# Optimization experiments

Hardware: AMD Instinct MI355X
Metric: run time of the kernel (lower is better)

Reference implementation:

```python
import jax, jax.numpy as jnp
import numpy as np

H = 24          # num_heads
QKV = 3 * 3072  # qkv_features * 3
EPS = 1e-6


def apply_rope(q, k, pe):
    # q,k: [B,H,L,D]; pe: [1,1,L,D//2,2,2]
    def rot(t):
        t_ = t.reshape(*t.shape[:-1], -1, 1, 2)  # [B,H,L,D/2,1,2]
        out = pe[..., 0] * t_[..., 0] + pe[..., 1] * t_[..., 1]  # [B,H,L,D/2,2]
        return out.reshape(t.shape)
    return rot(q), rot(k)


def setup_inputs() -> dict:
    key = jax.random.key(0)
    ks = jax.random.split(key, 8)
    B, L, D, Dh = 1, 2048, 3072, 128
    s = lambda n: 1.0 / np.sqrt(n)
    return {
        "x": jax.random.normal(ks[0], (B, L, D), jnp.float32),
        "vec": jax.random.normal(ks[1], (B, D), jnp.float32),
        "pe": jax.random.normal(ks[2], (1, 1, L, Dh // 2, 2, 2), jnp.float32),
        "w_mod": jax.random.normal(ks[3], (D, 3 * D), jnp.float32) * s(D),
        "b_mod": jnp.zeros((3 * D,), jnp.float32),
        "w1": jax.random.normal(ks[4], (D, QKV + 4 * D), jnp.float32) * s(D),
        "b1": jnp.zeros((QKV + 4 * D,), jnp.float32),
        "w2": jax.random.normal(ks[5], (D + 4 * D, D), jnp.float32) * s(5 * D),
        "b2": jnp.zeros((D,), jnp.float32),
        "q_scale": jnp.ones((Dh,), jnp.float32),
        "k_scale": jnp.ones((Dh,), jnp.float32),
    }


def reference(x, vec, pe, w_mod, b_mod, w1, b1, w2, b2, q_scale, k_scale):
    B, L, D = x.shape
    # modulation: silu + linear -> shift, scale, gate each [B,1,D]
    m = jax.nn.silu(vec) @ w_mod + b_mod
    shift, scale, gate = [t[:, None, :] for t in jnp.split(m, 3, axis=-1)]
    # pre-norm (LayerNorm, no scale/bias) + modulate
    mu = jnp.mean(x, axis=-1, keepdims=True)
    var = jnp.mean((x - mu) ** 2, axis=-1, keepdims=True)
    xn = (x - mu) * jax.lax.rsqrt(var + EPS)
    x_mod = (1.0 + scale) * xn + shift
    # fused qkv + mlp projection
    h = x_mod @ w1 + b1
    qkv, mlp = h[..., :QKV], h[..., QKV:]
    qkv = qkv.reshape(B, L, 3, H, -1).transpose(2, 0, 3, 1, 4)  # [3,B,H,L,Dh]
    q, k, v = qkv[0], qkv[1], qkv[2]
    # QK RMSNorm
    rms = lambda t, g: t * jax.lax.rsqrt(jnp.mean(t * t, axis=-1, keepdims=True) + EPS) * g
    q, k = rms(q, q_scale), rms(k, k_scale)
    # RoPE
    q, k = apply_rope(q, k, pe)
    # attention
    Dh = q.shape[-1]
    logits = jnp.einsum("bhqd,bhkd->bhqk", q, k) * (Dh ** -0.5)
    attn = jnp.einsum("bhqk,bhkd->bhqd", jax.nn.softmax(logits, axis=-1), v)
    attn = attn.transpose(0, 2, 1, 3).reshape(B, L, H * Dh)
    # parallel gated MLP + output projection
    out = jnp.concatenate((attn, jax.nn.gelu(mlp)), axis=-1) @ w2 + b2
    return x + gate * out
```

## Files before the change

### kernel.cpp

```cpp
#include <hip/hip_runtime.h>

typedef __bf16 bf16;
typedef __bf16 bf16x8 __attribute__((ext_vector_type(8)));
typedef float f32x4 __attribute__((ext_vector_type(4)));

#define L_SEQ   2048
#define D_MODEL 3072
#define N_HEADS 24
#define N1      21504
#define QKV_N   9216
#define CC      15360


__device__ __forceinline__ void async_cp16(const void* g, void* s) {
    __builtin_amdgcn_global_load_lds((const __attribute__((address_space(1))) void*)g,
                                     (__attribute__((address_space(3))) void*)s, 16, 0, 0);
}

__global__ __launch_bounds__(256) void mod_init_kernel(const float* __restrict__ b_mod, float* __restrict__ m) {
    int j = blockIdx.x * 256 + threadIdx.x;
    m[j] = b_mod[j];
}

__global__ __launch_bounds__(256) void mod_gemv_kernel(const float* __restrict__ vec,
                                                       const float* __restrict__ w_mod,
                                                       float* __restrict__ m) {
    int j  = blockIdx.x * 256 + threadIdx.x;
    int d0 = blockIdx.y * 256;
    __shared__ float sv[256];
    float x = vec[d0 + threadIdx.x];
    sv[threadIdx.x] = x / (1.f + __expf(-x));
    __syncthreads();
    float acc = 0.f;
    #pragma unroll 8
    for (int d = 0; d < 256; d++)
        acc += sv[d] * w_mod[(size_t)(d0 + d) * QKV_N + j];
    atomicAdd(&m[j], acc);
}

__global__ __launch_bounds__(256) void ln_kernel(const float* __restrict__ x,
                                                 const float* __restrict__ m,
                                                 bf16* __restrict__ x_mod) {
    int l = blockIdx.x, tid = threadIdx.x;
    const float4* xr = (const float4*)(x + (size_t)l * D_MODEL);
    float4 v[3];
    float s = 0.f, ss = 0.f;
    #pragma unroll
    for (int p = 0; p < 3; p++) {
        v[p] = xr[p * 256 + tid];
        s  += v[p].x + v[p].y + v[p].z + v[p].w;
        ss += v[p].x * v[p].x + v[p].y * v[p].y + v[p].z * v[p].z + v[p].w * v[p].w;
    }
    #pragma unroll
    for (int off = 32; off; off >>= 1) { s += __shfl_xor(s, off); ss += __shfl_xor(ss, off); }
    __shared__ float rs[4], rss[4];
    int wave = tid >> 6, lane = tid & 63;
    if (lane == 0) { rs[wave] = s; rss[wave] = ss; }
    __syncthreads();
    s  = rs[0] + rs[1] + rs[2] + rs[3];
    ss = rss[0] + rss[1] + rss[2] + rss[3];
    float mu   = s * (1.f / D_MODEL);
    float var  = ss * (1.f / D_MODEL) - mu * mu;
    float rstd = rsqrtf(var + 1e-6f);
    #pragma unroll
    for (int p = 0; p < 3; p++) {
        int c = (p * 256 + tid) * 4;
        const float* ve = (const float*)&v[p];
        union { bf16 b[4]; uint2 u; } pk;
        #pragma unroll
        for (int e = 0; e < 4; e++) {
            float xn = (ve[e] - mu) * rstd;
            pk.b[e] = (bf16)((1.f + m[D_MODEL + c + e]) * xn + m[c + e]);
        }
        *(uint2*)(x_mod + (size_t)l * D_MODEL + c) = pk.u;
    }
}

__global__ __launch_bounds__(256) void tconv_kernel(const float* __restrict__ in, bf16* __restrict__ out,
                                                    int R, int C) {
    __shared__ float T[64][65];
    int c0 = blockIdx.x * 64, r0 = blockIdx.y * 64;
    int tid = threadIdx.x;
    int col4 = (tid & 15) * 4, rr = tid >> 4;
    #pragma unroll
    for (int p = 0; p < 4; p++) {
        int r = rr + p * 16;
        float4 v = *(const float4*)(in + (size_t)(r0 + r) * C + c0 + col4);
        T[r][col4 + 0] = v.x; T[r][col4 + 1] = v.y; T[r][col4 + 2] = v.z; T[r][col4 + 3] = v.w;
    }
    __syncthreads();
    int c = tid >> 2, rq = (tid & 3) * 16;
    union { bf16 b[16]; uint4 u[2]; } pk;
    #pragma unroll
    for (int i = 0; i < 16; i++) pk.b[i] = (bf16)T[rq + i][c];
    uint4* op = (uint4*)(out + (size_t)(c0 + c) * R + r0 + rq);
    op[0] = pk.u[0]; op[1] = pk.u[1];
}

template <int EPI>
__global__ __launch_bounds__(256) void gemm_kernel(
    const bf16* __restrict__ A, const bf16* __restrict__ Bt,
    const float* __restrict__ bias, int K, int ld,
    bf16* __restrict__ o_qkv, bf16* __restrict__ o_concat,
    float* __restrict__ p0, float* __restrict__ p1) {
    __shared__ bf16 As[128 * 32];
    __shared__ bf16 Bs[128 * 32];
    const int tid = threadIdx.x;
    const int wave = tid >> 6, lane = tid & 63;
    const int l16 = lane & 15, lq = lane >> 4;
    const int wm = (wave >> 1) * 64, wn = (wave & 1) * 64;
    const int m0 = blockIdx.y * 128, n0 = blockIdx.x * 128;
    const int koff = (EPI == 2) ? blockIdx.z * K : 0;

    const int srow  = wave * 16 + (lane >> 2);
    const int skoff = (lane & 3) * 8;
    const bf16* Ag = A  + (size_t)(m0 + srow) * ld + koff + skoff;
    const bf16* Bg = Bt + (size_t)(n0 + srow) * ld + koff + skoff;
    bf16* As_w = As + wave * 16 * 32;
    bf16* Bs_w = Bs + wave * 16 * 32;

    f32x4 acc[4][4];
    #pragma unroll
    for (int i = 0; i < 4; i++)
        #pragma unroll
        for (int j = 0; j < 4; j++) acc[i][j] = f32x4{0.f, 0.f, 0.f, 0.f};

    for (int k0 = 0; k0 < K; k0 += 32) {
        __syncthreads();
        async_cp16(Ag + k0,                    As_w);
        async_cp16(Ag + k0 + (size_t)64 * ld,  As_w + 64 * 32);
        async_cp16(Bg + k0,                    Bs_w);
        async_cp16(Bg + k0 + (size_t)64 * ld,  Bs_w + 64 * 32);
        __syncthreads();
        bf16x8 af[4], bfr[4];
        #pragma unroll
        for (int i = 0; i < 4; i++) af[i]  = *(const bf16x8*)(As + (wm + 16 * i + l16) * 32 + lq * 8);
        #pragma unroll
        for (int j = 0; j < 4; j++) bfr[j] = *(const bf16x8*)(Bs + (wn + 16 * j + l16) * 32 + lq * 8);
        #pragma unroll
        for (int i = 0; i < 4; i++)
            #pragma unroll
            for (int j = 0; j < 4; j++)
                acc[i][j] = __builtin_amdgcn_mfma_f32_16x16x32_bf16(af[i], bfr[j], acc[i][j], 0, 0, 0);
    }

    float* po = (EPI == 2) ? (blockIdx.z ? p1 : p0) : nullptr;
    #pragma unroll
    for (int i = 0; i < 4; i++) {
        int row = m0 + wm + 16 * i + lq * 4;
        #pragma unroll
        for (int j = 0; j < 4; j++) {
            int col = n0 + wn + 16 * j + l16;
            float bv = (EPI == 1) ? bias[col] : 0.f;
            #pragma unroll
            for (int r = 0; r < 4; r++) {
                float v = acc[i][j][r] + bv;
                int rr = row + r;
                if (EPI == 1) {
                    if (col < QKV_N) {
                        o_qkv[(size_t)rr * QKV_N + col] = (bf16)v;
                    } else {
                        float g = 0.5f * v * (1.f + tanhf(0.7978845608028654f * (v + 0.044715f * v * v * v)));
                        o_concat[(size_t)rr * CC + (col - QKV_N + D_MODEL)] = (bf16)g;
                    }
                } else {
                    po[(size_t)rr * D_MODEL + col] = v;
                }
            }
        }
    }
}

__global__ __launch_bounds__(256) void res_kernel(const float* __restrict__ p0, const float* __restrict__ p1,
                                                  const float* __restrict__ x, const float* __restrict__ gate,
                                                  const float* __restrict__ b2, float* __restrict__ out) {
    int i = blockIdx.x * 256 + threadIdx.x;
    float4 a  = ((const float4*)p0)[i];
    float4 b  = ((const float4*)p1)[i];
    float4 xr = ((const float4*)x)[i];
    int col = (i * 4) % D_MODEL;
    float4 g  = *(const float4*)(gate + col);
    float4 bb = *(const float4*)(b2 + col);
    float4 o;
    o.x = xr.x + g.x * (a.x + b.x + bb.x);
    o.y = xr.y + g.y * (a.y + b.y + bb.y);
    o.z = xr.z + g.z * (a.z + b.z + bb.z);
    o.w = xr.w + g.w * (a.w + b.w + bb.w);
    ((float4*)out)[i] = o;
}

__global__ __launch_bounds__(256) void qkv_rope_kernel(const bf16* __restrict__ hqkv,
                                                       const float* __restrict__ pe,
                                                       const float* __restrict__ q_scale,
                                                       const float* __restrict__ k_scale,
                                                       bf16* __restrict__ q_r, bf16* __restrict__ k_r) {
    int wave = threadIdx.x >> 6, lane = threadIdx.x & 63;
    int idx = blockIdx.x * 4 + wave;
    int l = idx / N_HEADS, h = idx - l * N_HEADS;
    const bf16* qg = hqkv + (size_t)l * QKV_N + h * 128;
    const bf16* kg = qg + D_MODEL;
    float q0 = (float)qg[2 * lane], q1 = (float)qg[2 * lane + 1];
    float k0 = (float)kg[2 * lane], k1 = (float)kg[2 * lane + 1];
    float sq = q0 * q0 + q1 * q1, sk = k0 * k0 + k1 * k1;
    #pragma unroll
    for (int off = 32; off; off >>= 1) { sq += __shfl_xor(sq, off); sk += __shfl_xor(sk, off); }
    float rq = rsqrtf(sq * (1.f / 128.f) + 1e-6f);
    float rk = rsqrtf(sk * (1.f / 128.f) + 1e-6f);
    float s0 = q_scale[2 * lane], s1 = q_scale[2 * lane + 1];
    float z0 = k_scale[2 * lane], z1 = k_scale[2 * lane + 1];
    float4 p = ((const float4*)pe)[(size_t)l * 64 + lane];
    float tq0 = q0 * rq * s0, tq1 = q1 * rq * s1;
    float tk0 = k0 * rk * z0, tk1 = k1 * rk * z1;
    size_t ob = ((size_t)h * L_SEQ + l) * 128 + 2 * lane;
    q_r[ob]     = (bf16)(p.x * tq0 + p.y * tq1);
    q_r[ob + 1] = (bf16)(p.z * tq0 + p.w * tq1);
    k_r[ob]     = (bf16)(p.x * tk0 + p.y * tk1);
    k_r[ob + 1] = (bf16)(p.z * tk0 + p.w * tk1);
}

__global__ __launch_bounds__(256) void vtrans_kernel(const bf16* __restrict__ hqkv, bf16* __restrict__ v_t) {
    int dt = blockIdx.x * 64, lt = blockIdx.y * 64, h = blockIdx.z;
    __shared__ bf16 T[64][72];
    int tid = threadIdx.x;
    #pragma unroll
    for (int p = 0; p < 2; p++) {
        int idx = p * 256 + tid;
        int r = idx >> 3, c = idx & 7;
        uint4 v = *(const uint4*)(hqkv + (size_t)(lt + r) * QKV_N + 2 * D_MODEL + h * 128 + dt + c * 8);
        *(uint4*)(&T[r][c * 8]) = v;
    }
    __syncthreads();
    #pragma unroll
    for (int p = 0; p < 2; p++) {
        int idx = p * 256 + tid;
        int d = idx >> 3, c = idx & 7;
        union { bf16 b[8]; uint4 u; } pk;
        #pragma unroll
        for (int i = 0; i < 8; i++) pk.b[i] = T[c * 8 + i][d];
        *(uint4*)(v_t + ((size_t)h * 128 + dt + d) * L_SEQ + lt + c * 8) = pk.u;
    }
}

#define QK_LD 136
#define VP_LD 72
__global__ __launch_bounds__(256) void attn_kernel(const bf16* __restrict__ q_r, const bf16* __restrict__ k_r,
                                                   const bf16* __restrict__ v_t, bf16* __restrict__ concat) {
    const int h = blockIdx.y;
    const int q0 = blockIdx.x * 64;
    __shared__ bf16 Qs[64 * QK_LD];
    __shared__ bf16 Ks[64 * QK_LD];
    __shared__ bf16 Vs[128 * VP_LD];
    __shared__ bf16 Ps[64 * VP_LD];
    const int tid = threadIdx.x, wave = tid >> 6, lane = tid & 63;
    const int l16 = lane & 15, lq = lane >> 4;
    const bf16* Qg = q_r + ((size_t)h * L_SEQ + q0) * 128;
    const bf16* Kg = k_r + (size_t)h * L_SEQ * 128;
    const bf16* Vg = v_t + (size_t)h * 128 * L_SEQ;
    #pragma unroll
    for (int p = 0; p < 4; p++) {
        int idx = p * 256 + tid, r = idx >> 4, c = idx & 15;
        *(uint4*)(Qs + r * QK_LD + c * 8) = *(const uint4*)(Qg + (size_t)r * 128 + c * 8);
    }
    f32x4 accO[8];
    #pragma unroll
    for (int i = 0; i < 8; i++) accO[i] = f32x4{0.f, 0.f, 0.f, 0.f};
    float mrow[4] = {-1e30f, -1e30f, -1e30f, -1e30f};
    float lrow[4] = {0.f, 0.f, 0.f, 0.f};
    const float sc = 0.08838834764831845f * 1.4426950408889634f;
    for (int kt = 0; kt < 32; kt++) {
        __syncthreads();
        const bf16* Kt = Kg + (size_t)kt * 64 * 128;
        const bf16* Vt = Vg + kt * 64;
        #pragma unroll
        for (int p = 0; p < 4; p++) {
            int idx = p * 256 + tid, r = idx >> 4, c = idx & 15;
            *(uint4*)(Ks + r * QK_LD + c * 8) = *(const uint4*)(Kt + (size_t)r * 128 + c * 8);
        }
        #pragma unroll
        for (int p = 0; p < 4; p++) {
            int idx = p * 256 + tid, r = idx >> 3, c = idx & 7;
            *(uint4*)(Vs + r * VP_LD + c * 8) = *(const uint4*)(Vt + (size_t)r * L_SEQ + c * 8);
        }
        __syncthreads();
        f32x4 accS[4];
        #pragma unroll
        for (int i = 0; i < 4; i++) accS[i] = f32x4{0.f, 0.f, 0.f, 0.f};
        #pragma unroll
        for (int kk = 0; kk < 4; kk++) {
            bf16x8 a = *(const bf16x8*)(Qs + (wave * 16 + l16) * QK_LD + kk * 32 + lq * 8);
            #pragma unroll
            for (int nt = 0; nt < 4; nt++) {
                bf16x8 b = *(const bf16x8*)(Ks + (nt * 16 + l16) * QK_LD + kk * 32 + lq * 8);
                accS[nt] = __builtin_amdgcn_mfma_f32_16x16x32_bf16(a, b, accS[nt], 0, 0, 0);
            }
        }
        float alpha[4];
        #pragma unroll
        for (int r = 0; r < 4; r++) {
            float x0 = accS[0][r] * sc, x1 = accS[1][r] * sc, x2 = accS[2][r] * sc, x3 = accS[3][r] * sc;
            float mx = fmaxf(fmaxf(x0, x1), fmaxf(x2, x3));
            #pragma unroll
            for (int off = 1; off < 16; off <<= 1) mx = fmaxf(mx, __shfl_xor(mx, off));
            float mnew = fmaxf(mrow[r], mx);
            alpha[r] = __builtin_amdgcn_exp2f(mrow[r] - mnew);
            float p0 = __builtin_amdgcn_exp2f(x0 - mnew), p1 = __builtin_amdgcn_exp2f(x1 - mnew);
            float p2 = __builtin_amdgcn_exp2f(x2 - mnew), p3 = __builtin_amdgcn_exp2f(x3 - mnew);
            float rsum = p0 + p1 + p2 + p3;
            #pragma unroll
            for (int off = 1; off < 16; off <<= 1) rsum += __shfl_xor(rsum, off);
            lrow[r] = lrow[r] * alpha[r] + rsum;
            mrow[r] = mnew;
            int prow = wave * 16 + lq * 4 + r;
            Ps[prow * VP_LD +  0 + l16] = (bf16)p0;
            Ps[prow * VP_LD + 16 + l16] = (bf16)p1;
            Ps[prow * VP_LD + 32 + l16] = (bf16)p2;
            Ps[prow * VP_LD + 48 + l16] = (bf16)p3;
        }
        #pragma unroll
        for (int i = 0; i < 8; i++) {
            accO[i][0] *= alpha[0]; accO[i][1] *= alpha[1];
            accO[i][2] *= alpha[2]; accO[i][3] *= alpha[3];
        }
        #pragma unroll
        for (int kk = 0; kk < 2; kk++) {
            bf16x8 a = *(const bf16x8*)(Ps + (wave * 16 + l16) * VP_LD + kk * 32 + lq * 8);
            #pragma unroll
            for (int nt = 0; nt < 8; nt++) {
                bf16x8 b = *(const bf16x8*)(Vs + (nt * 16 + l16) * VP_LD + kk * 32 + lq * 8);
                accO[nt] = __builtin_amdgcn_mfma_f32_16x16x32_bf16(a, b, accO[nt], 0, 0, 0);
            }
        }
    }
    float inv[4];
    #pragma unroll
    for (int r = 0; r < 4; r++) inv[r] = 1.f / lrow[r];
    #pragma unroll
    for (int nt = 0; nt < 8; nt++)
        #pragma unroll
        for (int r = 0; r < 4; r++) {
            int row = q0 + wave * 16 + lq * 4 + r;
            concat[(size_t)row * CC + h * 128 + nt * 16 + l16] = (bf16)(accO[nt][r] * inv[r]);
        }
}

extern "C" void kernel_launch(void* const* d_in, const int* in_sizes, int n_in,
                              void* d_out, int out_size, void* d_ws, size_t ws_size,
                              hipStream_t stream) {
    const float* x       = (const float*)d_in[0];
    const float* vec     = (const float*)d_in[1];
    const float* pe      = (const float*)d_in[2];
    const float* w_mod   = (const float*)d_in[3];
    const float* b_mod   = (const float*)d_in[4];
    const float* w1      = (const float*)d_in[5];
    const float* b1      = (const float*)d_in[6];
    const float* w2      = (const float*)d_in[7];
    const float* b2      = (const float*)d_in[8];
    const float* q_scale = (const float*)d_in[9];
    const float* k_scale = (const float*)d_in[10];
    float* out = (float*)d_out;

    char* ws = (char*)d_ws;
    float* m_buf  = (float*)(ws);
    bf16* x_mod   = (bf16*)(ws + 36864);
    bf16* w1t     = (bf16*)(ws + 12619776);
    bf16* hqkv    = (bf16*)(ws + 144740352);
    bf16* concat  = (bf16*)(ws + 182489088);
    bf16* q_r     = (bf16*)(ws + 245403648);
    bf16* k_r     = (bf16*)(ws + 257986560);
    bf16* v_t     = (bf16*)(ws + 270569472);
    float* p0     = (float*)(ws + 144740352);
    float* p1     = (float*)(ws + 245403648);

    mod_init_kernel<<<36, 256, 0, stream>>>(b_mod, m_buf);
    mod_gemv_kernel<<<dim3(36, 12), 256, 0, stream>>>(vec, w_mod, m_buf);
    ln_kernel<<<L_SEQ, 256, 0, stream>>>(x, m_buf, x_mod);
    tconv_kernel<<<dim3(N1 / 64, D_MODEL / 64), 256, 0, stream>>>(w1, w1t, D_MODEL, N1);
    gemm_kernel<1><<<dim3(N1 / 128, L_SEQ / 128, 1), 256, 0, stream>>>(
        x_mod, w1t, b1, D_MODEL, D_MODEL, hqkv, concat, nullptr, nullptr);
    qkv_rope_kernel<<<L_SEQ * N_HEADS / 4, 256, 0, stream>>>(hqkv, pe, q_scale, k_scale, q_r, k_r);
    vtrans_kernel<<<dim3(2, 32, N_HEADS), 256, 0, stream>>>(hqkv, v_t);
    attn_kernel<<<dim3(32, N_HEADS), 256, 0, stream>>>(q_r, k_r, v_t, concat);
    tconv_kernel<<<dim3(D_MODEL / 64, CC / 64), 256, 0, stream>>>(w2, w1t, CC, D_MODEL);
    gemm_kernel<2><<<dim3(D_MODEL / 128, L_SEQ / 128, 2), 256, 0, stream>>>(
        concat, w1t, nullptr, CC / 2, CC, nullptr, nullptr, p0, p1);
    res_kernel<<<L_SEQ * D_MODEL / 1024, 256, 0, stream>>>(p0, p1, x, m_buf + 2 * D_MODEL, b2, out);
}
```

Before: 1.449 ms.

## Use 32x32x16 MFMA with BK=64 XOR-swizzled LDS in GEMM; keep Q in registers

The GEMM kernel moves from 16x16x32 to 32x32x16 bf16 MFMA tiles, doubles the K step to 64 and XOR-swizzles the LDS layout to avoid bank conflicts, with launch bounds asking for 3 blocks per CU. The aim is fewer LDS reads per MFMA and half as many barriers per K. Separately, the attention kernel loads its Q fragments straight into registers and drops the Q shared-memory tile. LDS use per GEMM block doubles, and the occupancy hint may force register spills.

```diff
diff --git a/kernel.cpp b/kernel.cpp
--- a/kernel.cpp
+++ b/kernel.cpp
@@ -3,6 +3,7 @@
 typedef __bf16 bf16;
 typedef __bf16 bf16x8 __attribute__((ext_vector_type(8)));
 typedef float f32x4 __attribute__((ext_vector_type(4)));
+typedef float f32x16 __attribute__((ext_vector_type(16)));
 
 #define L_SEQ   2048
 #define D_MODEL 3072
@@ -98,64 +99,71 @@
 }
 
 template <int EPI>
-__global__ __launch_bounds__(256) void gemm_kernel(
+__global__ __launch_bounds__(256, 3) void gemm_kernel(
     const bf16* __restrict__ A, const bf16* __restrict__ Bt,
     const float* __restrict__ bias, int K, int ld,
     bf16* __restrict__ o_qkv, bf16* __restrict__ o_concat,
     float* __restrict__ p0, float* __restrict__ p1) {
-    __shared__ bf16 As[128 * 32];
-    __shared__ bf16 Bs[128 * 32];
+    __shared__ bf16 As[128 * 64];
+    __shared__ bf16 Bs[128 * 64];
     const int tid = threadIdx.x;
     const int wave = tid >> 6, lane = tid & 63;
-    const int l16 = lane & 15, lq = lane >> 4;
+    const int l32 = lane & 31, lh = lane >> 5;
     const int wm = (wave >> 1) * 64, wn = (wave & 1) * 64;
     const int m0 = blockIdx.y * 128, n0 = blockIdx.x * 128;
     const int koff = (EPI == 2) ? blockIdx.z * K : 0;
 
-    const int srow  = wave * 16 + (lane >> 2);
-    const int skoff = (lane & 3) * 8;
-    const bf16* Ag = A  + (size_t)(m0 + srow) * ld + koff + skoff;
-    const bf16* Bg = Bt + (size_t)(n0 + srow) * ld + koff + skoff;
-    bf16* As_w = As + wave * 16 * 32;
-    bf16* Bs_w = Bs + wave * 16 * 32;
-
-    f32x4 acc[4][4];
-    #pragma unroll
-    for (int i = 0; i < 4; i++)
-        #pragma unroll
-        for (int j = 0; j < 4; j++) acc[i][j] = f32x4{0.f, 0.f, 0.f, 0.f};
-
-    for (int k0 = 0; k0 < K; k0 += 32) {
+    const int srow_i  = lane >> 3;
+    const int schunk  = (lane & 7) ^ srow_i;
+    const bf16* Agl = A  + (size_t)(m0 + wave * 8 + srow_i) * ld + koff + schunk * 8;
+    const bf16* Bgl = Bt + (size_t)(n0 + wave * 8 + srow_i) * ld + koff + schunk * 8;
+    bf16* As_w = As + wave * 8 * 64;
+    bf16* Bs_w = Bs + wave * 8 * 64;
+
+    f32x16 acc[2][2];
+    #pragma unroll
+    for (int i = 0; i < 2; i++)
+        #pragma unroll
+        for (int j = 0; j < 2; j++)
+            #pragma unroll
+            for (int e = 0; e < 16; e++) acc[i][j][e] = 0.f;
+
+    const int sw = l32 & 7;
+
+    for (int k0 = 0; k0 < K; k0 += 64) {
         __syncthreads();
-        async_cp16(Ag + k0,                    As_w);
-        async_cp16(Ag + k0 + (size_t)64 * ld,  As_w + 64 * 32);
-        async_cp16(Bg + k0,                    Bs_w);
-        async_cp16(Bg + k0 + (size_t)64 * ld,  Bs_w + 64 * 32);
+        #pragma unroll
+        for (int i = 0; i < 4; i++) {
+            async_cp16(Agl + k0 + (size_t)(i * 32) * ld, As_w + i * 32 * 64);
+            async_cp16(Bgl + k0 + (size_t)(i * 32) * ld, Bs_w + i * 32 * 64);
+        }
         __syncthreads();
-        bf16x8 af[4], bfr[4];
-        #pragma unroll
-        for (int i = 0; i < 4; i++) af[i]  = *(const bf16x8*)(As + (wm + 16 * i + l16) * 32 + lq * 8);
-        #pragma unroll
-        for (int j = 0; j < 4; j++) bfr[j] = *(const bf16x8*)(Bs + (wn + 16 * j + l16) * 32 + lq * 8);
-        #pragma unroll
-        for (int i = 0; i < 4; i++)
-            #pragma unroll
-            for (int j = 0; j < 4; j++)
-                acc[i][j] = __builtin_amdgcn_mfma_f32_16x16x32_bf16(af[i], bfr[j], acc[i][j], 0, 0, 0);
+        #pragma unroll
+        for (int ks = 0; ks < 4; ks++) {
+            const int pos = ((ks * 2 + lh) ^ sw) * 8;
+            bf16x8 a0 = *(const bf16x8*)(As + (wm +      l32) * 64 + pos);
+            bf16x8 a1 = *(const bf16x8*)(As + (wm + 32 + l32) * 64 + pos);
+            bf16x8 b0 = *(const bf16x8*)(Bs + (wn +      l32) * 64 + pos);
+            bf16x8 b1 = *(const bf16x8*)(Bs + (wn + 32 + l32) * 64 + pos);
+            acc[0][0] = __builtin_amdgcn_mfma_f32_32x32x16_bf16(a0, b0, acc[0][0], 0, 0, 0);
+            acc[0][1] = __builtin_amdgcn_mfma_f32_32x32x16_bf16(a0, b1, acc[0][1], 0, 0, 0);
+            acc[1][0] = __builtin_amdgcn_mfma_f32_32x32x16_bf16(a1, b0, acc[1][0], 0, 0, 0);
+            acc[1][1] = __builtin_amdgcn_mfma_f32_32x32x16_bf16(a1, b1, acc[1][1], 0, 0, 0);
+        }
     }
 
     float* po = (EPI == 2) ? (blockIdx.z ? p1 : p0) : nullptr;
     #pragma unroll
-    for (int i = 0; i < 4; i++) {
-        int row = m0 + wm + 16 * i + lq * 4;
-        #pragma unroll
-        for (int j = 0; j < 4; j++) {
-            int col = n0 + wn + 16 * j + l16;
+    for (int mt = 0; mt < 2; mt++) {
+        #pragma unroll
+        for (int nt = 0; nt < 2; nt++) {
+            int col = n0 + wn + nt * 32 + l32;
+            int rbase = m0 + wm + mt * 32 + 4 * lh;
             float bv = (EPI == 1) ? bias[col] : 0.f;
             #pragma unroll
-            for (int r = 0; r < 4; r++) {
-                float v = acc[i][j][r] + bv;
-                int rr = row + r;
+            for (int r = 0; r < 16; r++) {
+                int rr = rbase + (r & 3) + 8 * (r >> 2);
+                float v = acc[mt][nt][r] + bv;
                 if (EPI == 1) {
                     if (col < QKV_N) {
                         o_qkv[(size_t)rr * QKV_N + col] = (bf16)v;
@@ -247,7 +255,6 @@
                                                    const bf16* __restrict__ v_t, bf16* __restrict__ concat) {
     const int h = blockIdx.y;
     const int q0 = blockIdx.x * 64;
-    __shared__ bf16 Qs[64 * QK_LD];
     __shared__ bf16 Ks[64 * QK_LD];
     __shared__ bf16 Vs[128 * VP_LD];
     __shared__ bf16 Ps[64 * VP_LD];
@@ -256,11 +263,10 @@
     const bf16* Qg = q_r + ((size_t)h * L_SEQ + q0) * 128;
     const bf16* Kg = k_r + (size_t)h * L_SEQ * 128;
     const bf16* Vg = v_t + (size_t)h * 128 * L_SEQ;
-    #pragma unroll
-    for (int p = 0; p < 4; p++) {
-        int idx = p * 256 + tid, r = idx >> 4, c = idx & 15;
-        *(uint4*)(Qs + r * QK_LD + c * 8) = *(const uint4*)(Qg + (size_t)r * 128 + c * 8);
-    }
+    bf16x8 aq[4];
+    #pragma unroll
+    for (int kk = 0; kk < 4; kk++)
+        aq[kk] = *(const bf16x8*)(Qg + (size_t)(wave * 16 + l16) * 128 + kk * 32 + lq * 8);
     f32x4 accO[8];
     #pragma unroll
     for (int i = 0; i < 8; i++) accO[i] = f32x4{0.f, 0.f, 0.f, 0.f};
@@ -287,11 +293,10 @@
         for (int i = 0; i < 4; i++) accS[i] = f32x4{0.f, 0.f, 0.f, 0.f};
         #pragma unroll
         for (int kk = 0; kk < 4; kk++) {
-            bf16x8 a = *(const bf16x8*)(Qs + (wave * 16 + l16) * QK_LD + kk * 32 + lq * 8);
             #pragma unroll
             for (int nt = 0; nt < 4; nt++) {
                 bf16x8 b = *(const bf16x8*)(Ks + (nt * 16 + l16) * QK_LD + kk * 32 + lq * 8);
-                accS[nt] = __builtin_amdgcn_mfma_f32_16x16x32_bf16(a, b, accS[nt], 0, 0, 0);
+                accS[nt] = __builtin_amdgcn_mfma_f32_16x16x32_bf16(aq[kk], b, accS[nt], 0, 0, 0);
             }
         }
         float alpha[4];
```

Result: faster. 1.324 ms (-8.6%).
